# Performance work log

Hardware: AMD Instinct MI355X
Metric: run time of the kernel (lower is better)

Reference implementation:

```python
import jax, jax.numpy as jnp
import numpy as np

NIN, NOUT, ES, HS, NL = 2, 2, 16, 16, 3
B, T = 4096, 512


def setup_inputs() -> dict:
    key = jax.random.key(0)
    ks = jax.random.split(key, 4 + 4 * NL)
    s_in = 1.0 / np.sqrt(NIN)
    s_es = 1.0 / np.sqrt(ES)
    s_hs = 1.0 / np.sqrt(HS)
    inp = {
        'x': jax.random.normal(ks[0], (B, T, NIN), dtype=jnp.float32),
        'h0': jnp.zeros((NL, B, HS), dtype=jnp.float32),
        'W_emb': jax.random.uniform(ks[1], (ES, NIN), minval=-s_in, maxval=s_in, dtype=jnp.float32),
        'b_emb': jnp.zeros((ES,), dtype=jnp.float32),
        'W_out': jax.random.uniform(ks[2], (NOUT, HS), minval=-s_hs, maxval=s_hs, dtype=jnp.float32),
        'b_out': jnp.zeros((NOUT,), dtype=jnp.float32),
    }
    for l in range(NL):
        in_dim = ES if l == 0 else HS
        k0, k1, k2, k3 = jax.random.split(ks[4 + l], 4)
        inp[f'W_ih{l}'] = jax.random.uniform(k0, (3 * HS, in_dim), minval=-s_hs, maxval=s_hs, dtype=jnp.float32)
        inp[f'W_hh{l}'] = jax.random.uniform(k1, (3 * HS, HS), minval=-s_hs, maxval=s_hs, dtype=jnp.float32)
        inp[f'b_ih{l}'] = jax.random.uniform(k2, (3 * HS,), minval=-s_hs, maxval=s_hs, dtype=jnp.float32)
        inp[f'b_hh{l}'] = jax.random.uniform(k3, (3 * HS,), minval=-s_hs, maxval=s_hs, dtype=jnp.float32)
    return inp


def _gru_layer(x_seq, h0, W_ih, b_ih, W_hh, b_hh):
    # Precompute input-side gates for all timesteps: [B, T, 3H]
    gx = jnp.einsum('bti,gi->btg', x_seq, W_ih) + b_ih

    def step(h, gx_t):
        gh = h @ W_hh.T + b_hh  # [B, 3H]
        xr, xz, xn = jnp.split(gx_t, 3, axis=-1)
        hr, hz, hn = jnp.split(gh, 3, axis=-1)
        r = jax.nn.sigmoid(xr + hr)
        z = jax.nn.sigmoid(xz + hz)
        n = jnp.tanh(xn + r * hn)
        h_new = (1.0 - z) * n + z * h
        return h_new, h_new

    hT, ys = jax.lax.scan(step, h0, gx.transpose(1, 0, 2))  # scan over T
    return ys.transpose(1, 0, 2), hT  # [B, T, H], [B, H]


def reference(x, h0, W_emb, b_emb, W_out, b_out,
              W_ih0, W_hh0, b_ih0, b_hh0,
              W_ih1, W_hh1, b_ih1, b_hh1,
              W_ih2, W_hh2, b_ih2, b_hh2):
    # Embedding linear + ReLU
    h = jax.nn.relu(jnp.einsum('bti,ei->bte', x, W_emb) + b_emb)  # [B, T, ES]
    layer_params = [
        (W_ih0, b_ih0, W_hh0, b_hh0),
        (W_ih1, b_ih1, W_hh1, b_hh1),
        (W_ih2, b_ih2, W_hh2, b_hh2),
    ]
    finals = []
    for l, (Wi, bi, Wh, bh) in enumerate(layer_params):
        h, hT = _gru_layer(h, h0[l], Wi, bi, Wh, bh)
        finals.append(hT)
    hidden = jnp.stack(finals, axis=0)  # [NL, B, HS]
    out = jnp.einsum('bth,oh->bto', h, W_out) + b_out  # [B, T, NOUT]
    return out, hidden
```

## Files before the change

### kernel.cpp

```cpp
#include <hip/hip_runtime.h>
#include <hip/hip_bf16.h>

#define TT 512
#define BB 4096

typedef __attribute__((ext_vector_type(4))) float f32x4;
typedef __attribute__((ext_vector_type(8))) _Float16 f16x8;
typedef __attribute__((ext_vector_type(4))) unsigned int uint4v;

__device__ __forceinline__ f32x4 MFMA16(f16x8 a, f16x8 b, f32x4 c) {
    return __builtin_amdgcn_mfma_f32_16x16x32_f16(a, b, c, 0, 0, 0);
}
__device__ __forceinline__ float fast_rcp(float x) { return __builtin_amdgcn_rcpf(x); }
__device__ __forceinline__ unsigned int pkdup(float a) {
    return __builtin_bit_cast(unsigned int, __builtin_amdgcn_cvt_pkrtz(a, a));
}

__global__ __launch_bounds__(256, 1)
void gru_p4f_kernel(const float* __restrict__ x, const float* __restrict__ h0,
                    const float* __restrict__ W_emb, const float* __restrict__ b_emb,
                    const float* __restrict__ W_out, const float* __restrict__ b_out,
                    const float* __restrict__ Wih0, const float* __restrict__ Whh0,
                    const float* __restrict__ bih0, const float* __restrict__ bhh0,
                    const float* __restrict__ Wih1, const float* __restrict__ Whh1,
                    const float* __restrict__ bih1, const float* __restrict__ bhh1,
                    const float* __restrict__ Wih2, const float* __restrict__ Whh2,
                    const float* __restrict__ bih2, const float* __restrict__ bhh2,
                    float* __restrict__ out)
{
    const int tid = threadIdx.x;
    const int wid = tid >> 6;
    const int l   = tid & 63;
    const int n   = l & 15;
    const int g   = l >> 4;
    const int b   = blockIdx.x * 16 + n;

    __shared__ uint4v lbuf[2][2][4][64];
    __shared__ f32x4  obuf[2][4][64];

    const int lw = wid < 3 ? wid : 2;
    const float* Wih = lw == 0 ? Wih0 : (lw == 1 ? Wih1 : Wih2);
    const float* Whh = lw == 0 ? Whh0 : (lw == 1 ? Whh1 : Whh2);
    const float* bih = lw == 0 ? bih0 : (lw == 1 ? bih1 : bih2);
    const float* bhh = lw == 0 ? bhh0 : (lw == 1 ? bhh1 : bhh2);

    f16x8 aX[3], aH[3];
#pragma unroll
    for (int gate = 0; gate < 3; ++gate) {
        const float ks = (gate == 2) ? -2.0f : -1.0f;
        f16x8 fx, fh;
#pragma unroll
        for (int q = 0; q < 4; ++q) {
            fx[2 * q]     = (_Float16)(ks * Wih[(gate * 16 + n) * 16 + 4 * g + q]);
            fx[2 * q + 1] = (_Float16)0.0f;
            fh[2 * q]     = (_Float16)(ks * Whh[(gate * 16 + n) * 16 + 4 * g + q]);
            fh[2 * q + 1] = (_Float16)0.0f;
        }
        aX[gate] = fx; aH[gate] = fh;
    }

    f32x4 bR, bZ, bNX, bNH;
#pragma unroll
    for (int j = 0; j < 4; ++j) {
        const int m = 4 * g + j;
        bR[j]  = -1.0f * (bih[m]      + bhh[m]);
        bZ[j]  = -1.0f * (bih[16 + m] + bhh[16 + m]);
        bNX[j] = -2.0f * bih[32 + m];
        bNH[j] = -2.0f * bhh[32 + m];
    }

    float wex[4], wey[4], beq[4];
#pragma unroll
    for (int q = 0; q < 4; ++q) {
        const int c = 4 * g + q;
        wex[q] = W_emb[c * 2]; wey[q] = W_emb[c * 2 + 1]; beq[q] = b_emb[c];
    }
    float wo0[4], wo1[4];
#pragma unroll
    for (int j = 0; j < 4; ++j) { wo0[j] = W_out[4 * g + j]; wo1[j] = W_out[16 + 4 * g + j]; }
    const float bo0 = b_out[0], bo1 = b_out[1];

    f32x4 hC = *(const f32x4*)(h0 + ((size_t)lw * BB + b) * 16 + 4 * g);
    uint4v hB4;
#pragma unroll
    for (int q = 0; q < 4; ++q) hB4[q] = pkdup(hC[q]);

    const float* xb = x + (size_t)b * (TT * 2);
    float4 xc0 = make_float4(0.f, 0.f, 0.f, 0.f), xc1 = xc0;
    if (wid == 0) { xc0 = *(const float4*)xb; xc1 = *(const float4*)(xb + 4); }

#define HB() __builtin_bit_cast(f16x8, hB4)

#define GATES(AR, AZ, ANH, ANX)                                           \
    do {                                                                  \
        _Pragma("unroll")                                                 \
        for (int j = 0; j < 4; ++j) {                                     \
            const float Er = __expf(AR[j]);                               \
            const float Ez = __expf(AZ[j]);                               \
            const float r  = fast_rcp(1.0f + Er);                         \
            const float En = __expf(fmaf(r, ANH[j], ANX[j]));             \
            const float num = fmaf(En, hC[j] - Ez, hC[j] + Ez);           \
            const float den = fmaf(En, Ez, En) + (1.0f + Ez);             \
            hC[j] = num * fast_rcp(den);                                  \
        }                                                                 \
        _Pragma("unroll")                                                 \
        for (int q = 0; q < 4; ++q) hB4[q] = pkdup(hC[q]);                \
    } while (0)

#define HANDOFF(i)                                                        \
    do {                                                                  \
        if (wid < 2) lbuf[s & 1][wid][i][l] = hB4;                        \
        else         obuf[s & 1][i][l] = hC;                              \
    } while (0)

    const int NS = TT / 4 + 3;
    for (int s = 0; s < NS; ++s) {
        const int t0 = 4 * (s - wid);
        if (t0 >= 0 && t0 < TT) {
            if (wid < 3) {
                f16x8 B0, B1, B2, B3;
                if (wid == 0) {
                    uint4v u0, u1, u2, u3;
#pragma unroll
                    for (int q = 0; q < 4; ++q) {
                        u0[q] = pkdup(fmaxf(fmaf(wey[q], xc0.y, fmaf(wex[q], xc0.x, beq[q])), 0.0f));
                        u1[q] = pkdup(fmaxf(fmaf(wey[q], xc0.w, fmaf(wex[q], xc0.z, beq[q])), 0.0f));
                        u2[q] = pkdup(fmaxf(fmaf(wey[q], xc1.y, fmaf(wex[q], xc1.x, beq[q])), 0.0f));
                        u3[q] = pkdup(fmaxf(fmaf(wey[q], xc1.w, fmaf(wex[q], xc1.z, beq[q])), 0.0f));
                    }
                    B0 = __builtin_bit_cast(f16x8, u0);
                    B1 = __builtin_bit_cast(f16x8, u1);
                    B2 = __builtin_bit_cast(f16x8, u2);
                    B3 = __builtin_bit_cast(f16x8, u3);
                    if (t0 + 4 < TT) {
                        xc0 = *(const float4*)(xb + (t0 + 4) * 2);
                        xc1 = *(const float4*)(xb + (t0 + 4) * 2 + 4);
                    }
                } else {
                    const int pp = (s - 1) & 1;
                    B0 = __builtin_bit_cast(f16x8, lbuf[pp][wid - 1][0][l]);
                    B1 = __builtin_bit_cast(f16x8, lbuf[pp][wid - 1][1][l]);
                    B2 = __builtin_bit_cast(f16x8, lbuf[pp][wid - 1][2][l]);
                    B3 = __builtin_bit_cast(f16x8, lbuf[pp][wid - 1][3][l]);
                }

                f32x4 arA  = MFMA16(aH[0], HB(), bR);
                f32x4 azA  = MFMA16(aH[1], HB(), bZ);
                f32x4 anhA = MFMA16(aH[2], HB(), bNH);
                f32x4 anxA = MFMA16(aX[2], B0, bNX);
                arA = MFMA16(aX[0], B0, arA);
                azA = MFMA16(aX[1], B0, azA);
                f32x4 arB  = MFMA16(aX[0], B1, bR);
                f32x4 azB  = MFMA16(aX[1], B1, bZ);
                f32x4 anxB = MFMA16(aX[2], B1, bNX);
                GATES(arA, azA, anhA, anxA);
                HANDOFF(0);
                f32x4 anhB = MFMA16(aH[2], HB(), bNH);
                arB = MFMA16(aH[0], HB(), arB);
                azB = MFMA16(aH[1], HB(), azB);
                arA  = MFMA16(aX[0], B2, bR);
                azA  = MFMA16(aX[1], B2, bZ);
                anxA = MFMA16(aX[2], B2, bNX);
                GATES(arB, azB, anhB, anxB);
                HANDOFF(1);
                anhA = MFMA16(aH[2], HB(), bNH);
                arA = MFMA16(aH[0], HB(), arA);
                azA = MFMA16(aH[1], HB(), azA);
                arB  = MFMA16(aX[0], B3, bR);
                azB  = MFMA16(aX[1], B3, bZ);
                anxB = MFMA16(aX[2], B3, bNX);
                GATES(arA, azA, anhA, anxA);
                HANDOFF(2);
                anhB = MFMA16(aH[2], HB(), bNH);
                arB = MFMA16(aH[0], HB(), arB);
                azB = MFMA16(aH[1], HB(), azB);
                GATES(arB, azB, anhB, anxB);
                HANDOFF(3);
            } else {
                const int pp = (s - 1) & 1;
                float pr[8];
#pragma unroll
                for (int i = 0; i < 4; ++i) {
                    const f32x4 h2 = obuf[pp][i][l];
                    float p0 = 0.f, p1 = 0.f;
#pragma unroll
                    for (int j = 0; j < 4; ++j) {
                        p0 = fmaf(wo0[j], h2[j], p0);
                        p1 = fmaf(wo1[j], h2[j], p1);
                    }
                    p0 += __shfl_xor(p0, 16); p0 += __shfl_xor(p0, 32);
                    p1 += __shfl_xor(p1, 16); p1 += __shfl_xor(p1, 32);
                    pr[2 * i] = p0 + bo0; pr[2 * i + 1] = p1 + bo1;
                }
                if (g == 0) {
                    float* op = out + (size_t)b * (TT * 2) + t0 * 2;
                    *(float4*)(op)     = make_float4(pr[0], pr[1], pr[2], pr[3]);
                    *(float4*)(op + 4) = make_float4(pr[4], pr[5], pr[6], pr[7]);
                }
            }
        }
        asm volatile("s_waitcnt lgkmcnt(0)\n\ts_barrier" ::: "memory");
    }

    if (wid < 3)
        *(f32x4*)(out + (size_t)BB * TT * 2 + ((size_t)wid * BB + b) * 16 + 4 * g) = hC;

#undef GATES
#undef HANDOFF
#undef HB
}

extern "C" void kernel_launch(void* const* d_in, const int* in_sizes, int n_in,
                              void* d_out, int out_size, void* d_ws, size_t ws_size,
                              hipStream_t stream) {
    const float* x     = (const float*)d_in[0];
    const float* h0    = (const float*)d_in[1];
    const float* W_emb = (const float*)d_in[2];
    const float* b_emb = (const float*)d_in[3];
    const float* W_out = (const float*)d_in[4];
    const float* b_out = (const float*)d_in[5];
    const float* Wih0  = (const float*)d_in[6];
    const float* Whh0  = (const float*)d_in[7];
    const float* bih0  = (const float*)d_in[8];
    const float* bhh0  = (const float*)d_in[9];
    const float* Wih1  = (const float*)d_in[10];
    const float* Whh1  = (const float*)d_in[11];
    const float* bih1  = (const float*)d_in[12];
    const float* bhh1  = (const float*)d_in[13];
    const float* Wih2  = (const float*)d_in[14];
    const float* Whh2  = (const float*)d_in[15];
    const float* bih2  = (const float*)d_in[16];
    const float* bhh2  = (const float*)d_in[17];
    float* out = (float*)d_out;

    gru_p4f_kernel<<<dim3(BB / 16), dim3(256), 0, stream>>>(
        x, h0, W_emb, b_emb, W_out, b_out,
        Wih0, Whh0, bih0, bhh0,
        Wih1, Whh1, bih1, bhh1,
        Wih2, Whh2, bih2, bhh2,
        out);
}
```

Before: 187.1 us.

## Process eight timesteps per pipeline stage and use exp2 with log2e-folded weights

Each wave now handles 8 timesteps per barrier-separated pipeline stage instead of 4, which halves the number of block-wide barriers and LDS handoff rounds and shortens the pipeline fill and drain. The MFMA schedule becomes a loop that interleaves the next step's input-side MFMAs with the current step's gate math. Separately, log2(e) is folded into the weights and biases so the gate activations can call the hardware exp2 directly instead of __expf. In exchange, LDS buffers double in size and register pressure rises from holding 8 B-operands and 4 x-loads.

```diff
diff --git a/kernel.cpp b/kernel.cpp
--- a/kernel.cpp
+++ b/kernel.cpp
@@ -12,21 +12,25 @@
     return __builtin_amdgcn_mfma_f32_16x16x32_f16(a, b, c, 0, 0, 0);
 }
 __device__ __forceinline__ float fast_rcp(float x) { return __builtin_amdgcn_rcpf(x); }
+__device__ __forceinline__ float fast_exp2(float x) { return __builtin_amdgcn_exp2f(x); }
 __device__ __forceinline__ unsigned int pkdup(float a) {
     return __builtin_bit_cast(unsigned int, __builtin_amdgcn_cvt_pkrtz(a, a));
 }
 
+#define KS1 (-1.44269504088896340736f)
+#define KS2 (-2.88539008177792681472f)
+
 __global__ __launch_bounds__(256, 1)
-void gru_p4f_kernel(const float* __restrict__ x, const float* __restrict__ h0,
-                    const float* __restrict__ W_emb, const float* __restrict__ b_emb,
-                    const float* __restrict__ W_out, const float* __restrict__ b_out,
-                    const float* __restrict__ Wih0, const float* __restrict__ Whh0,
-                    const float* __restrict__ bih0, const float* __restrict__ bhh0,
-                    const float* __restrict__ Wih1, const float* __restrict__ Whh1,
-                    const float* __restrict__ bih1, const float* __restrict__ bhh1,
-                    const float* __restrict__ Wih2, const float* __restrict__ Whh2,
-                    const float* __restrict__ bih2, const float* __restrict__ bhh2,
-                    float* __restrict__ out)
+void gru_p8_kernel(const float* __restrict__ x, const float* __restrict__ h0,
+                   const float* __restrict__ W_emb, const float* __restrict__ b_emb,
+                   const float* __restrict__ W_out, const float* __restrict__ b_out,
+                   const float* __restrict__ Wih0, const float* __restrict__ Whh0,
+                   const float* __restrict__ bih0, const float* __restrict__ bhh0,
+                   const float* __restrict__ Wih1, const float* __restrict__ Whh1,
+                   const float* __restrict__ bih1, const float* __restrict__ bhh1,
+                   const float* __restrict__ Wih2, const float* __restrict__ Whh2,
+                   const float* __restrict__ bih2, const float* __restrict__ bhh2,
+                   float* __restrict__ out)
 {
     const int tid = threadIdx.x;
     const int wid = tid >> 6;
@@ -35,8 +39,8 @@
     const int g   = l >> 4;
     const int b   = blockIdx.x * 16 + n;
 
-    __shared__ uint4v lbuf[2][2][4][64];
-    __shared__ f32x4  obuf[2][4][64];
+    __shared__ uint4v lbuf[2][2][8][64];
+    __shared__ f32x4  obuf[2][8][64];
 
     const int lw = wid < 3 ? wid : 2;
     const float* Wih = lw == 0 ? Wih0 : (lw == 1 ? Wih1 : Wih2);
@@ -47,7 +51,7 @@
     f16x8 aX[3], aH[3];
 #pragma unroll
     for (int gate = 0; gate < 3; ++gate) {
-        const float ks = (gate == 2) ? -2.0f : -1.0f;
+        const float ks = (gate == 2) ? KS2 : KS1;
         f16x8 fx, fh;
 #pragma unroll
         for (int q = 0; q < 4; ++q) {
@@ -63,10 +67,10 @@
 #pragma unroll
     for (int j = 0; j < 4; ++j) {
         const int m = 4 * g + j;
-        bR[j]  = -1.0f * (bih[m]      + bhh[m]);
-        bZ[j]  = -1.0f * (bih[16 + m] + bhh[16 + m]);
-        bNX[j] = -2.0f * bih[32 + m];
-        bNH[j] = -2.0f * bhh[32 + m];
+        bR[j]  = KS1 * (bih[m]      + bhh[m]);
+        bZ[j]  = KS1 * (bih[16 + m] + bhh[16 + m]);
+        bNX[j] = KS2 * bih[32 + m];
+        bNH[j] = KS2 * bhh[32 + m];
     }
 
     float wex[4], wey[4], beq[4];
@@ -86,8 +90,11 @@
     for (int q = 0; q < 4; ++q) hB4[q] = pkdup(hC[q]);
 
     const float* xb = x + (size_t)b * (TT * 2);
-    float4 xc0 = make_float4(0.f, 0.f, 0.f, 0.f), xc1 = xc0;
-    if (wid == 0) { xc0 = *(const float4*)xb; xc1 = *(const float4*)(xb + 4); }
+    float4 xc[4];
+    if (wid == 0) {
+#pragma unroll
+        for (int q = 0; q < 4; ++q) xc[q] = *(const float4*)(xb + 4 * q);
+    }
 
 #define HB() __builtin_bit_cast(f16x8, hB4)
 
@@ -95,10 +102,10 @@
     do {                                                                  \
         _Pragma("unroll")                                                 \
         for (int j = 0; j < 4; ++j) {                                     \
-            const float Er = __expf(AR[j]);                               \
-            const float Ez = __expf(AZ[j]);                               \
+            const float Er = fast_exp2(AR[j]);                            \
+            const float Ez = fast_exp2(AZ[j]);                            \
             const float r  = fast_rcp(1.0f + Er);                         \
-            const float En = __expf(fmaf(r, ANH[j], ANX[j]));             \
+            const float En = fast_exp2(fmaf(r, ANH[j], ANX[j]));          \
             const float num = fmaf(En, hC[j] - Ez, hC[j] + Ez);           \
             const float den = fmaf(En, Ez, En) + (1.0f + Ez);             \
             hC[j] = num * fast_rcp(den);                                  \
@@ -113,89 +120,84 @@
         else         obuf[s & 1][i][l] = hC;                              \
     } while (0)
 
-    const int NS = TT / 4 + 3;
+    const int NS = TT / 8 + 3;
     for (int s = 0; s < NS; ++s) {
-        const int t0 = 4 * (s - wid);
+        const int t0 = 8 * (s - wid);
         if (t0 >= 0 && t0 < TT) {
             if (wid < 3) {
-                f16x8 B0, B1, B2, B3;
+                f16x8 Bv[8];
                 if (wid == 0) {
-                    uint4v u0, u1, u2, u3;
-#pragma unroll
-                    for (int q = 0; q < 4; ++q) {
-                        u0[q] = pkdup(fmaxf(fmaf(wey[q], xc0.y, fmaf(wex[q], xc0.x, beq[q])), 0.0f));
-                        u1[q] = pkdup(fmaxf(fmaf(wey[q], xc0.w, fmaf(wex[q], xc0.z, beq[q])), 0.0f));
-                        u2[q] = pkdup(fmaxf(fmaf(wey[q], xc1.y, fmaf(wex[q], xc1.x, beq[q])), 0.0f));
-                        u3[q] = pkdup(fmaxf(fmaf(wey[q], xc1.w, fmaf(wex[q], xc1.z, beq[q])), 0.0f));
-                    }
-                    B0 = __builtin_bit_cast(f16x8, u0);
-                    B1 = __builtin_bit_cast(f16x8, u1);
-                    B2 = __builtin_bit_cast(f16x8, u2);
-                    B3 = __builtin_bit_cast(f16x8, u3);
-                    if (t0 + 4 < TT) {
-                        xc0 = *(const float4*)(xb + (t0 + 4) * 2);
-                        xc1 = *(const float4*)(xb + (t0 + 4) * 2 + 4);
+#pragma unroll
+                    for (int i = 0; i < 4; ++i) {
+                        uint4v ua, ub;
+#pragma unroll
+                        for (int q = 0; q < 4; ++q) {
+                            ua[q] = pkdup(fmaxf(fmaf(wey[q], xc[i].y, fmaf(wex[q], xc[i].x, beq[q])), 0.0f));
+                            ub[q] = pkdup(fmaxf(fmaf(wey[q], xc[i].w, fmaf(wex[q], xc[i].z, beq[q])), 0.0f));
+                        }
+                        Bv[2 * i]     = __builtin_bit_cast(f16x8, ua);
+                        Bv[2 * i + 1] = __builtin_bit_cast(f16x8, ub);
+                    }
+                    if (t0 + 8 < TT) {
+#pragma unroll
+                        for (int q = 0; q < 4; ++q)
+                            xc[q] = *(const float4*)(xb + (t0 + 8) * 2 + 4 * q);
                     }
                 } else {
                     const int pp = (s - 1) & 1;
-                    B0 = __builtin_bit_cast(f16x8, lbuf[pp][wid - 1][0][l]);
-                    B1 = __builtin_bit_cast(f16x8, lbuf[pp][wid - 1][1][l]);
-                    B2 = __builtin_bit_cast(f16x8, lbuf[pp][wid - 1][2][l]);
-                    B3 = __builtin_bit_cast(f16x8, lbuf[pp][wid - 1][3][l]);
+#pragma unroll
+                    for (int i = 0; i < 8; ++i)
+                        Bv[i] = __builtin_bit_cast(f16x8, lbuf[pp][wid - 1][i][l]);
                 }
 
-                f32x4 arA  = MFMA16(aH[0], HB(), bR);
-                f32x4 azA  = MFMA16(aH[1], HB(), bZ);
-                f32x4 anhA = MFMA16(aH[2], HB(), bNH);
-                f32x4 anxA = MFMA16(aX[2], B0, bNX);
-                arA = MFMA16(aX[0], B0, arA);
-                azA = MFMA16(aX[1], B0, azA);
-                f32x4 arB  = MFMA16(aX[0], B1, bR);
-                f32x4 azB  = MFMA16(aX[1], B1, bZ);
-                f32x4 anxB = MFMA16(aX[2], B1, bNX);
-                GATES(arA, azA, anhA, anxA);
-                HANDOFF(0);
-                f32x4 anhB = MFMA16(aH[2], HB(), bNH);
-                arB = MFMA16(aH[0], HB(), arB);
-                azB = MFMA16(aH[1], HB(), azB);
-                arA  = MFMA16(aX[0], B2, bR);
-                azA  = MFMA16(aX[1], B2, bZ);
-                anxA = MFMA16(aX[2], B2, bNX);
-                GATES(arB, azB, anhB, anxB);
-                HANDOFF(1);
-                anhA = MFMA16(aH[2], HB(), bNH);
-                arA = MFMA16(aH[0], HB(), arA);
-                azA = MFMA16(aH[1], HB(), azA);
-                arB  = MFMA16(aX[0], B3, bR);
-                azB  = MFMA16(aX[1], B3, bZ);
-                anxB = MFMA16(aX[2], B3, bNX);
-                GATES(arA, azA, anhA, anxA);
-                HANDOFF(2);
-                anhB = MFMA16(aH[2], HB(), bNH);
-                arB = MFMA16(aH[0], HB(), arB);
-                azB = MFMA16(aH[1], HB(), azB);
-                GATES(arB, azB, anhB, anxB);
-                HANDOFF(3);
+                f32x4 arA = MFMA16(aX[0], Bv[0], bR);
+                f32x4 azA = MFMA16(aX[1], Bv[0], bZ);
+                f32x4 axA = MFMA16(aX[2], Bv[0], bNX);
+                f32x4 arB, azB, axB, anh;
+#pragma unroll
+                for (int i = 0; i < 8; i += 2) {
+                    anh = MFMA16(aH[2], HB(), bNH);
+                    arA = MFMA16(aH[0], HB(), arA);
+                    azA = MFMA16(aH[1], HB(), azA);
+                    arB = MFMA16(aX[0], Bv[i + 1], bR);
+                    azB = MFMA16(aX[1], Bv[i + 1], bZ);
+                    axB = MFMA16(aX[2], Bv[i + 1], bNX);
+                    GATES(arA, azA, anh, axA);
+                    HANDOFF(i);
+                    anh = MFMA16(aH[2], HB(), bNH);
+                    arB = MFMA16(aH[0], HB(), arB);
+                    azB = MFMA16(aH[1], HB(), azB);
+                    if (i + 2 < 8) {
+                        arA = MFMA16(aX[0], Bv[i + 2], bR);
+                        azA = MFMA16(aX[1], Bv[i + 2], bZ);
+                        axA = MFMA16(aX[2], Bv[i + 2], bNX);
+                    }
+                    GATES(arB, azB, anh, axB);
+                    HANDOFF(i + 1);
+                }
             } else {
                 const int pp = (s - 1) & 1;
-                float pr[8];
-#pragma unroll
-                for (int i = 0; i < 4; ++i) {
-                    const f32x4 h2 = obuf[pp][i][l];
-                    float p0 = 0.f, p1 = 0.f;
-#pragma unroll
-                    for (int j = 0; j < 4; ++j) {
-                        p0 = fmaf(wo0[j], h2[j], p0);
-                        p1 = fmaf(wo1[j], h2[j], p1);
-                    }
-                    p0 += __shfl_xor(p0, 16); p0 += __shfl_xor(p0, 32);
-                    p1 += __shfl_xor(p1, 16); p1 += __shfl_xor(p1, 32);
-                    pr[2 * i] = p0 + bo0; pr[2 * i + 1] = p1 + bo1;
-                }
-                if (g == 0) {
-                    float* op = out + (size_t)b * (TT * 2) + t0 * 2;
-                    *(float4*)(op)     = make_float4(pr[0], pr[1], pr[2], pr[3]);
-                    *(float4*)(op + 4) = make_float4(pr[4], pr[5], pr[6], pr[7]);
+#pragma unroll
+                for (int h = 0; h < 2; ++h) {
+                    float pr[8];
+#pragma unroll
+                    for (int i = 0; i < 4; ++i) {
+                        const f32x4 h2 = obuf[pp][4 * h + i][l];
+                        float p0 = 0.f, p1 = 0.f;
+#pragma unroll
+                        for (int j = 0; j < 4; ++j) {
+                            p0 = fmaf(wo0[j], h2[j], p0);
+                            p1 = fmaf(wo1[j], h2[j], p1);
+                        }
+                        p0 += __shfl_xor(p0, 16); p0 += __shfl_xor(p0, 32);
+                        p1 += __shfl_xor(p1, 16); p1 += __shfl_xor(p1, 32);
+                        pr[2 * i] = p0 + bo0; pr[2 * i + 1] = p1 + bo1;
+                    }
+                    if (g == 0) {
+                        float* op = out + (size_t)b * (TT * 2) + (t0 + 4 * h) * 2;
+                        *(float4*)(op)     = make_float4(pr[0], pr[1], pr[2], pr[3]);
+                        *(float4*)(op + 4) = make_float4(pr[4], pr[5], pr[6], pr[7]);
+                    }
                 }
             }
         }
@@ -233,7 +235,7 @@
     const float* bhh2  = (const float*)d_in[17];
     float* out = (float*)d_out;
 
-    gru_p4f_kernel<<<dim3(BB / 16), dim3(256), 0, stream>>>(
+    gru_p8_kernel<<<dim3(BB / 16), dim3(256), 0, stream>>>(
         x, h0, W_emb, b_emb, W_out, b_out,
         Wih0, Whh0, bih0, bhh0,
         Wih1, Whh1, bih1, bhh1,
```

Measured after the change: 160.6 us, median of 2. 1.16x faster.
